# Performance work log

Hardware: AMD Instinct MI355X
Metric: run time of the kernel (lower is better)

The kernel has to match this reference:

```python
import jax, jax.numpy as jnp
import numpy as np

B, S, D, E, K = 2, 2048, 512, 8, 2
H = 4 * D  # 2048


def setup_inputs() -> dict:
    key = jax.random.key(0)
    ks = jax.random.split(key, 6)
    x = jax.random.normal(ks[0], (B, S, D), dtype=jnp.float32)
    # parameters, matching torch init (randn weights, zero biases)
    w1 = jax.random.normal(ks[1], (E, D, H), dtype=jnp.float32)
    w2 = jax.random.normal(ks[2], (E, H, D), dtype=jnp.float32)
    b1 = jnp.zeros((E, H), dtype=jnp.float32)
    b2 = jnp.zeros((E, D), dtype=jnp.float32)
    # nn.Linear(D, E): kaiming-uniform-ish; plain uniform is fine for a baseline
    lim = 1.0 / np.sqrt(D)
    router_w = jax.random.uniform(ks[3], (D, E), dtype=jnp.float32, minval=-lim, maxval=lim)
    router_b = jax.random.uniform(ks[4], (E,), dtype=jnp.float32, minval=-lim, maxval=lim)
    return {"x": x, "w1": w1, "w2": w2, "b1": b1, "b2": b2,
            "router_w": router_w, "router_b": router_b}


def reference(x, w1, w2, b1, b2, router_w, router_b):
    # router: [b,s,e]
    router_logits = jnp.einsum('bsd,de->bse', x, router_w) + router_b
    top_k_logits, top_k_indices = jax.lax.top_k(router_logits, K)   # [b,s,k]
    top_k_probs = jax.nn.softmax(top_k_logits, axis=-1)             # [b,s,k]
    masks = jax.nn.one_hot(top_k_indices, E, dtype=x.dtype)          # [b,s,k,e]
    # dense all-expert MLP (faithful to source: every expert on every token)
    h = jnp.einsum('bsd,edh->bseh', x, w1) + b1                      # [b,s,e,4d]
    h = jax.nn.gelu(h, approximate=False)                            # exact gelu
    y = jnp.einsum('bseh,ehd->bsed', h, w2) + b2                     # [b,s,e,d]
    # combine: mask each expert output by routed prob and sum over top-k
    out = jnp.einsum('bsed,bske,bsk->bsd', y, masks, top_k_probs)    # [b,s,d]
    return out
```

## Files before the change

### kernel.cpp

```cpp
#include <hip/hip_runtime.h>
#include <math.h>

typedef unsigned short u16;
typedef __bf16 bf16x8 __attribute__((ext_vector_type(8)));
typedef float f32x4 __attribute__((ext_vector_type(4)));

#define T_TOKENS 4096
#define D_DIM    512
#define H_DIM    2048
#define E_NUM    8
#define CAP      4096
#define NSLOT    (T_TOKENS * 2)

__device__ __forceinline__ u16 f2bf(float f) {
  unsigned int u = __builtin_bit_cast(unsigned int, f);
  u = (u + 0x7fffu + ((u >> 16) & 1u)) >> 16;
  return (u16)u;
}

__device__ __forceinline__ void gload16(const void* g, void* l) {
  __builtin_amdgcn_global_load_lds(
      (__attribute__((address_space(1))) void*)(g),
      (__attribute__((address_space(3))) void*)(l), 16, 0, 0);
}

__device__ __forceinline__ float gelu_fast(float v) {
  float u = v * __fmaf_rn(0.071354817f, v * v, 1.59576912f);
  float e = __expf(-u);
  return v * __builtin_amdgcn_rcpf(1.0f + e);
}

__global__ __launch_bounds__(256) void transpose_both_kernel(const float* __restrict__ w1,
                                                             const float* __restrict__ w2,
                                                             u16* __restrict__ w1t,
                                                             u16* __restrict__ w2t) {
  __shared__ float tile[64][67];
  int bid = blockIdx.x;
  const float* in; u16* out; int R, C;
  if (bid < 2048) { in = w1; out = w1t; R = D_DIM; C = H_DIM; }
  else            { bid -= 2048; in = w2; out = w2t; R = H_DIM; C = D_DIM; }
  const int e = bid >> 8;
  const int t = bid & 255;
  const int nCx = C >> 6;
  const int c0 = (t % nCx) * 64, r0 = (t / nCx) * 64;
  const float* src = in + (size_t)e * D_DIM * H_DIM;
  u16* dst = out + (size_t)e * D_DIM * H_DIM;
  const int tid = threadIdx.x;
  {
    const int row = tid >> 2, cc = (tid & 3) * 16;
    const float* s = src + (size_t)(r0 + row) * C + c0 + cc;
#pragma unroll
    for (int j = 0; j < 4; j++)
      *(float4*)(&tile[row][cc + 4 * j]) = *(const float4*)(s + 4 * j);
  }
  __syncthreads();
  {
    const int c = tid >> 2, rc = (tid & 3) * 16;
    u16 buf[16];
#pragma unroll
    for (int j = 0; j < 16; j++) buf[j] = f2bf(tile[rc + j][c]);
    u16* d = dst + (size_t)(c0 + c) * R + r0 + rc;
    *(uint4*)(d)     = *(uint4*)(&buf[0]);
    *(uint4*)(d + 8) = *(uint4*)(&buf[8]);
  }
}

__global__ __launch_bounds__(256) void router_kernel(const float* __restrict__ x,
                                                     const float* __restrict__ rw,
                                                     const float* __restrict__ rb,
                                                     int* __restrict__ topk_idx,
                                                     float* __restrict__ topk_p,
                                                     u16* __restrict__ xb,
                                                     float* __restrict__ outz) {
  {
    float4 z = {0.f, 0.f, 0.f, 0.f};
    float4* o = (float4*)(outz + (size_t)blockIdx.x * 2048);
    o[threadIdx.x] = z;
    o[threadIdx.x + 256] = z;
  }
  const int lane = threadIdx.x & 63;
  const int t = blockIdx.x * 4 + (threadIdx.x >> 6);
  const float* xr = x + (size_t)t * D_DIM + lane * 8;
  float xv[8];
  *(float4*)(&xv[0]) = *(const float4*)(xr);
  *(float4*)(&xv[4]) = *(const float4*)(xr + 4);
  ushort4 o0, o1;
  o0.x = f2bf(xv[0]); o0.y = f2bf(xv[1]); o0.z = f2bf(xv[2]); o0.w = f2bf(xv[3]);
  o1.x = f2bf(xv[4]); o1.y = f2bf(xv[5]); o1.z = f2bf(xv[6]); o1.w = f2bf(xv[7]);
  ushort4* xo = (ushort4*)(xb + (size_t)t * D_DIM + lane * 8);
  xo[0] = o0; xo[1] = o1;

  float acc[8] = {0.f,0.f,0.f,0.f,0.f,0.f,0.f,0.f};
#pragma unroll
  for (int j = 0; j < 8; j++) {
    const float4* w = (const float4*)(rw + (size_t)(lane * 8 + j) * E_NUM);
    float4 w0 = w[0], w1 = w[1];
    acc[0] += xv[j] * w0.x; acc[1] += xv[j] * w0.y;
    acc[2] += xv[j] * w0.z; acc[3] += xv[j] * w0.w;
    acc[4] += xv[j] * w1.x; acc[5] += xv[j] * w1.y;
    acc[6] += xv[j] * w1.z; acc[7] += xv[j] * w1.w;
  }
#pragma unroll
  for (int off = 32; off > 0; off >>= 1) {
#pragma unroll
    for (int e = 0; e < 8; e++) acc[e] += __shfl_down(acc[e], off);
  }
  if (lane == 0) {
    float l[8];
#pragma unroll
    for (int e = 0; e < 8; e++) l[e] = acc[e] + rb[e];
    int i0 = 0; float v0 = l[0];
#pragma unroll
    for (int e = 1; e < 8; e++) if (l[e] > v0) { v0 = l[e]; i0 = e; }
    int i1 = -1; float v1 = -3.4e38f;
#pragma unroll
    for (int e = 0; e < 8; e++) if (e != i0 && l[e] > v1) { v1 = l[e]; i1 = e; }
    float p1 = expf(v1 - v0);
    float s = 1.0f + p1;
    topk_idx[t * 2] = i0; topk_idx[t * 2 + 1] = i1;
    topk_p[t * 2] = 1.0f / s; topk_p[t * 2 + 1] = p1 / s;
  }
}

__global__ __launch_bounds__(256) void compact_kernel(const int* __restrict__ topk_idx,
                                                      const float* __restrict__ topk_p,
                                                      int* __restrict__ slot_list,
                                                      float* __restrict__ prob_list,
                                                      int* __restrict__ counts) {
  const int e = blockIdx.x;
  const int tid = threadIdx.x, lane = tid & 63, w = tid >> 6;
  __shared__ int wsum[4];
  __shared__ int sbase;
  if (tid == 0) sbase = 0;
  __syncthreads();
  for (int c0 = 0; c0 < T_TOKENS; c0 += 256) {
    const int t = c0 + tid;
    const int i0 = topk_idx[t * 2], i1 = topk_idx[t * 2 + 1];
    int flag = 0, slot = 0; float p = 0.f;
    if (i0 == e)      { flag = 1; slot = t * 2;     p = topk_p[t * 2]; }
    else if (i1 == e) { flag = 1; slot = t * 2 + 1; p = topk_p[t * 2 + 1]; }
    unsigned long long m = __ballot(flag);
    if (lane == 0) wsum[w] = (int)__popcll(m);
    const int wpre = (int)__popcll(m & ((1ull << lane) - 1ull));
    __syncthreads();
    int base = sbase;
#pragma unroll
    for (int j = 0; j < 4; j++) if (j < w) base += wsum[j];
    const int tot = wsum[0] + wsum[1] + wsum[2] + wsum[3];
    if (flag) { slot_list[e * CAP + base + wpre] = slot; prob_list[e * CAP + base + wpre] = p; }
    __syncthreads();
    if (tid == 0) sbase += tot;
  }
  __syncthreads();
  if (tid == 0) counts[e] = sbase;
}

__global__ __launch_bounds__(256, 2) void gemm1_kernel(const u16* __restrict__ xb,
                                                       const u16* __restrict__ w1t,
                                                       const float* __restrict__ b1,
                                                       const int* __restrict__ slot_list,
                                                       const float* __restrict__ prob_list,
                                                       const int* __restrict__ counts,
                                                       u16* __restrict__ hbuf) {
  const int e  = blockIdx.y >> 5;
  const int rt = blockIdx.y & 31;
  const int cnt = counts[e];
  const int rbase = rt * 128;
  if (rbase >= cnt) return;
  const int n0 = blockIdx.x * 128;

  __shared__ __align__(16) u16 At[2][128 * 64];
  __shared__ __align__(16) u16 Bt[2][128 * 64];

  const int tid = threadIdx.x, lane = tid & 63, wid = tid >> 6;
  const int wr = wid >> 1, wc = wid & 1;
  const int lr8 = lane >> 3;
  const int sx = lane & 7;
  const int kperm = (sx ^ lr8) * 8;
  const int lrow = lane & 15, lk = lane >> 4;

  const u16* pa[4]; const u16* pb[4]; int lo[4];
#pragma unroll
  for (int i = 0; i < 4; i++) {
    const int row = (wid * 4 + i) * 8 + lr8;
    const int grow = rbase + row;
    int tok = 0;
    if (grow < cnt) tok = slot_list[e * CAP + grow] >> 1;
    pa[i] = xb + (size_t)tok * D_DIM + kperm;
    pb[i] = w1t + ((size_t)e * H_DIM + n0 + row) * D_DIM + kperm;
    lo[i] = (wid * 4 + i) * 512;
  }

  f32x4 acc[4][4];
#pragma unroll
  for (int i = 0; i < 4; i++)
#pragma unroll
    for (int j = 0; j < 4; j++) acc[i][j] = (f32x4){0.f, 0.f, 0.f, 0.f};

  auto stage = [&](int k0, int b) {
#pragma unroll
    for (int i = 0; i < 4; i++) gload16(pa[i] + k0, &At[b][lo[i]]);
#pragma unroll
    for (int i = 0; i < 4; i++) gload16(pb[i] + k0, &Bt[b][lo[i]]);
  };

  stage(0, 0);
  stage(64, 1);
  const int nt = D_DIM / 64;
#pragma unroll
  for (int t = 0; t < nt; ++t) {
    const int cur = t & 1;
    if (t < nt - 1) { asm volatile("s_waitcnt vmcnt(8)" ::: "memory"); }
    else            { asm volatile("s_waitcnt vmcnt(0)" ::: "memory"); }
    __builtin_amdgcn_sched_barrier(0);
    __builtin_amdgcn_s_barrier();
    bf16x8 afr[4][2], bfr[4][2];
#pragma unroll
    for (int ks = 0; ks < 2; ks++)
#pragma unroll
      for (int f = 0; f < 4; f++) {
        afr[f][ks] = *(const bf16x8*)(&At[cur][(wr * 64 + f * 16 + lrow) * 64 + ((ks * 4 + lk) ^ sx) * 8]);
        bfr[f][ks] = *(const bf16x8*)(&Bt[cur][(wc * 64 + f * 16 + lrow) * 64 + ((ks * 4 + lk) ^ sx) * 8]);
      }
    asm volatile("s_waitcnt lgkmcnt(0)" ::: "memory");
    __builtin_amdgcn_sched_barrier(0);
    __builtin_amdgcn_s_barrier();
    if (t + 2 < nt) stage((t + 2) * 64, cur);
    __builtin_amdgcn_sched_barrier(0);
    __builtin_amdgcn_s_setprio(1);
#pragma unroll
    for (int ks = 0; ks < 2; ks++)
#pragma unroll
      for (int fr = 0; fr < 4; fr++)
#pragma unroll
        for (int fc = 0; fc < 4; fc++)
          acc[fr][fc] = __builtin_amdgcn_mfma_f32_16x16x32_bf16(afr[fr][ks], bfr[fc][ks], acc[fr][fc], 0, 0, 0);
    __builtin_amdgcn_s_setprio(0);
  }

  float bias[4];
#pragma unroll
  for (int fc = 0; fc < 4; fc++) bias[fc] = b1[e * H_DIM + n0 + wc * 64 + fc * 16 + lrow];
#pragma unroll
  for (int fr = 0; fr < 4; fr++) {
#pragma unroll
    for (int reg = 0; reg < 4; reg++) {
      const int rloc = wr * 64 + fr * 16 + lk * 4 + reg;
      const int grow = rbase + rloc;
      if (grow < cnt) {
        const int slot = slot_list[e * CAP + grow];
        const float p  = prob_list[e * CAP + grow];
        u16* dst = hbuf + (size_t)slot * H_DIM + n0 + wc * 64 + lrow;
#pragma unroll
        for (int fc = 0; fc < 4; fc++) {
          float v = acc[fr][fc][reg] + bias[fc];
          dst[fc * 16] = f2bf(gelu_fast(v) * p);
        }
      }
    }
  }
}

__global__ __launch_bounds__(256, 3) void gemm2_kernel(const u16* __restrict__ hbuf,
                                                       const u16* __restrict__ w2t,
                                                       const float* __restrict__ b2,
                                                       const int* __restrict__ slot_list,
                                                       const float* __restrict__ prob_list,
                                                       const int* __restrict__ counts,
                                                       float* __restrict__ out) {
  const int e  = blockIdx.y >> 6;
  const int rt = blockIdx.y & 63;
  const int cnt = counts[e];
  const int rbase = rt * 64;
  if (rbase >= cnt) return;
  const int n0 = blockIdx.x * 128;

  __shared__ __align__(16) u16 At[2][64 * 64];
  __shared__ __align__(16) u16 Bt[2][128 * 64];

  const int tid = threadIdx.x, lane = tid & 63, wid = tid >> 6;
  const int wr = wid >> 1, wc = wid & 1;
  const int lr8 = lane >> 3;
  const int sx = lane & 7;
  const int kperm = (sx ^ lr8) * 8;
  const int lrow = lane & 15, lk = lane >> 4;

  const u16* pa[2]; int loa[2];
#pragma unroll
  for (int i = 0; i < 2; i++) {
    const int row = (wid * 2 + i) * 8 + lr8;
    const int grow = rbase + row;
    int slot = 0;
    if (grow < cnt) slot = slot_list[e * CAP + grow];
    pa[i] = hbuf + (size_t)slot * H_DIM + kperm;
    loa[i] = (wid * 2 + i) * 512;
  }
  const u16* pb[4]; int lob[4];
#pragma unroll
  for (int i = 0; i < 4; i++) {
    const int row = (wid * 4 + i) * 8 + lr8;
    pb[i] = w2t + ((size_t)e * D_DIM + n0 + row) * H_DIM + kperm;
    lob[i] = (wid * 4 + i) * 512;
  }

  f32x4 acc[2][4];
#pragma unroll
  for (int i = 0; i < 2; i++)
#pragma unroll
    for (int j = 0; j < 4; j++) acc[i][j] = (f32x4){0.f, 0.f, 0.f, 0.f};

  auto stage = [&](int k0, int b) {
#pragma unroll
    for (int i = 0; i < 2; i++) gload16(pa[i] + k0, &At[b][loa[i]]);
#pragma unroll
    for (int i = 0; i < 4; i++) gload16(pb[i] + k0, &Bt[b][lob[i]]);
  };

  stage(0, 0);
  stage(64, 1);
  const int nt = H_DIM / 64;
#pragma unroll 2
  for (int t = 0; t < nt; ++t) {
    const int cur = t & 1;
    if (t < nt - 1) { asm volatile("s_waitcnt vmcnt(6)" ::: "memory"); }
    else            { asm volatile("s_waitcnt vmcnt(0)" ::: "memory"); }
    __builtin_amdgcn_sched_barrier(0);
    __builtin_amdgcn_s_barrier();
    bf16x8 afr[2][2], bfr[4][2];
#pragma unroll
    for (int ks = 0; ks < 2; ks++) {
#pragma unroll
      for (int f = 0; f < 2; f++)
        afr[f][ks] = *(const bf16x8*)(&At[cur][(wr * 32 + f * 16 + lrow) * 64 + ((ks * 4 + lk) ^ sx) * 8]);
#pragma unroll
      for (int f = 0; f < 4; f++)
        bfr[f][ks] = *(const bf16x8*)(&Bt[cur][(wc * 64 + f * 16 + lrow) * 64 + ((ks * 4 + lk) ^ sx) * 8]);
    }
    asm volatile("s_waitcnt lgkmcnt(0)" ::: "memory");
    __builtin_amdgcn_sched_barrier(0);
    __builtin_amdgcn_s_barrier();
    if (t + 2 < nt) stage((t + 2) * 64, cur);
    __builtin_amdgcn_sched_barrier(0);
    __builtin_amdgcn_s_setprio(1);
#pragma unroll
    for (int ks = 0; ks < 2; ks++)
#pragma unroll
      for (int fr = 0; fr < 2; fr++)
#pragma unroll
        for (int fc = 0; fc < 4; fc++)
          acc[fr][fc] = __builtin_amdgcn_mfma_f32_16x16x32_bf16(afr[fr][ks], bfr[fc][ks], acc[fr][fc], 0, 0, 0);
    __builtin_amdgcn_s_setprio(0);
  }

#pragma unroll
  for (int fr = 0; fr < 2; fr++) {
#pragma unroll
    for (int reg = 0; reg < 4; reg++) {
      const int rloc = wr * 32 + fr * 16 + lk * 4 + reg;
      const int grow = rbase + rloc;
      if (grow < cnt) {
        const int slot = slot_list[e * CAP + grow];
        const float p  = prob_list[e * CAP + grow];
        float* dst = out + (size_t)(slot >> 1) * D_DIM + n0 + wc * 64 + lrow;
#pragma unroll
        for (int fc = 0; fc < 4; fc++) {
          float v = acc[fr][fc][reg] + p * b2[e * D_DIM + n0 + wc * 64 + fc * 16 + lrow];
          atomicAdd(&dst[fc * 16], v);
        }
      }
    }
  }
}

extern "C" void kernel_launch(void* const* d_in, const int* in_sizes, int n_in,
                              void* d_out, int out_size, void* d_ws, size_t ws_size,
                              hipStream_t stream) {
  const float* x  = (const float*)d_in[0];
  const float* w1 = (const float*)d_in[1];
  const float* w2 = (const float*)d_in[2];
  const float* b1 = (const float*)d_in[3];
  const float* b2 = (const float*)d_in[4];
  const float* rw = (const float*)d_in[5];
  const float* rb = (const float*)d_in[6];
  float* out = (float*)d_out;

  char* ws = (char*)d_ws;
  size_t off = 0;
  auto alloc = [&](size_t bytes) -> void* {
    void* p = ws + off;
    off = (off + bytes + 255) & ~(size_t)255;
    return p;
  };
  int*   counts    = (int*)alloc(E_NUM * 4);
  int*   slot_list = (int*)alloc((size_t)E_NUM * CAP * 4);
  float* prob_list = (float*)alloc((size_t)E_NUM * CAP * 4);
  int*   topk_idx  = (int*)alloc((size_t)T_TOKENS * 2 * 4);
  float* topk_p    = (float*)alloc((size_t)T_TOKENS * 2 * 4);
  u16*   xb        = (u16*)alloc((size_t)T_TOKENS * D_DIM * 2);
  u16*   w1t       = (u16*)alloc((size_t)E_NUM * H_DIM * D_DIM * 2);
  u16*   w2t       = (u16*)alloc((size_t)E_NUM * H_DIM * D_DIM * 2);
  u16*   hbuf      = (u16*)alloc((size_t)NSLOT * H_DIM * 2);

  transpose_both_kernel<<<4096, 256, 0, stream>>>(w1, w2, w1t, w2t);
  router_kernel<<<T_TOKENS / 4, 256, 0, stream>>>(x, rw, rb, topk_idx, topk_p, xb, out);
  compact_kernel<<<E_NUM, 256, 0, stream>>>(topk_idx, topk_p, slot_list, prob_list, counts);
  gemm1_kernel<<<dim3(H_DIM / 128, E_NUM * 32), 256, 0, stream>>>(xb, w1t, b1, slot_list, prob_list, counts, hbuf);
  gemm2_kernel<<<dim3(D_DIM / 128, E_NUM * 64), 256, 0, stream>>>(hbuf, w2t, b2, slot_list, prob_list, counts, out);
}
```

Measured before the change: 129.0 us.

## Parallelize expert compaction and retile expert GEMMs with triple-buffered pipelines

The serial per-expert compaction kernel is replaced by a chunked count pass plus a parallel scatter pass, so 128 blocks share the work instead of 8 blocks each looping over all tokens. gemm1 moves to 64-row tiles. Both GEMMs get a 3-stage LDS pipeline and a flattened 1D grid that interleaves experts across consecutive blocks. The aim is to cut the serial compaction time, improve load balance across experts and hide more memory latency, at the cost of an extra launch, more LDS per block and lower occupancy for gemm2 (launch bounds 3→2).

Measured after the change: 145.2 us. 12.6% more time.

```diff
diff --git a/kernel.cpp b/kernel.cpp
--- a/kernel.cpp
+++ b/kernel.cpp
@@ -11,6 +11,7 @@
 #define E_NUM    8
 #define CAP      4096
 #define NSLOT    (T_TOKENS * 2)
+#define NCHUNK   16
 
 __device__ __forceinline__ u16 f2bf(float f) {
   unsigned int u = __builtin_bit_cast(unsigned int, f);
@@ -122,37 +123,48 @@
   }
 }
 
-__global__ __launch_bounds__(256) void compact_kernel(const int* __restrict__ topk_idx,
+__global__ __launch_bounds__(256) void count_kernel(const int* __restrict__ topk_idx,
+                                                    int* __restrict__ chunkcnt) {
+  const int b = blockIdx.x, tid = threadIdx.x, lane = tid & 63, w = tid >> 6;
+  const int t = b * 256 + tid;
+  const int i0 = topk_idx[t * 2], i1 = topk_idx[t * 2 + 1];
+  __shared__ int ws[4][E_NUM];
+#pragma unroll
+  for (int e = 0; e < E_NUM; e++) {
+    unsigned long long m = __ballot(i0 == e || i1 == e);
+    if (lane == 0) ws[w][e] = (int)__popcll(m);
+  }
+  __syncthreads();
+  if (tid < E_NUM)
+    chunkcnt[b * E_NUM + tid] = ws[0][tid] + ws[1][tid] + ws[2][tid] + ws[3][tid];
+}
+
+__global__ __launch_bounds__(256) void scatter_kernel(const int* __restrict__ topk_idx,
                                                       const float* __restrict__ topk_p,
+                                                      const int* __restrict__ chunkcnt,
                                                       int* __restrict__ slot_list,
                                                       float* __restrict__ prob_list,
                                                       int* __restrict__ counts) {
-  const int e = blockIdx.x;
+  const int e = blockIdx.x & 7, chunk = blockIdx.x >> 3;
   const int tid = threadIdx.x, lane = tid & 63, w = tid >> 6;
+  int base = 0;
+  for (int c = 0; c < chunk; ++c) base += chunkcnt[c * E_NUM + e];
+  const int t = chunk * 256 + tid;
+  const int i0 = topk_idx[t * 2], i1 = topk_idx[t * 2 + 1];
+  int flag = 0, slot = 0; float p = 0.f;
+  if (i0 == e)      { flag = 1; slot = t * 2;     p = topk_p[t * 2]; }
+  else if (i1 == e) { flag = 1; slot = t * 2 + 1; p = topk_p[t * 2 + 1]; }
+  unsigned long long m = __ballot(flag);
   __shared__ int wsum[4];
-  __shared__ int sbase;
-  if (tid == 0) sbase = 0;
+  if (lane == 0) wsum[w] = (int)__popcll(m);
+  const int wpre = (int)__popcll(m & ((1ull << lane) - 1ull));
   __syncthreads();
-  for (int c0 = 0; c0 < T_TOKENS; c0 += 256) {
-    const int t = c0 + tid;
-    const int i0 = topk_idx[t * 2], i1 = topk_idx[t * 2 + 1];
-    int flag = 0, slot = 0; float p = 0.f;
-    if (i0 == e)      { flag = 1; slot = t * 2;     p = topk_p[t * 2]; }
-    else if (i1 == e) { flag = 1; slot = t * 2 + 1; p = topk_p[t * 2 + 1]; }
-    unsigned long long m = __ballot(flag);
-    if (lane == 0) wsum[w] = (int)__popcll(m);
-    const int wpre = (int)__popcll(m & ((1ull << lane) - 1ull));
-    __syncthreads();
-    int base = sbase;
-#pragma unroll
-    for (int j = 0; j < 4; j++) if (j < w) base += wsum[j];
-    const int tot = wsum[0] + wsum[1] + wsum[2] + wsum[3];
-    if (flag) { slot_list[e * CAP + base + wpre] = slot; prob_list[e * CAP + base + wpre] = p; }
-    __syncthreads();
-    if (tid == 0) sbase += tot;
-  }
-  __syncthreads();
-  if (tid == 0) counts[e] = sbase;
+  int wb = base;
+#pragma unroll
+  for (int j = 0; j < 4; j++) if (j < w) wb += wsum[j];
+  if (flag) { slot_list[e * CAP + wb + wpre] = slot; prob_list[e * CAP + wb + wpre] = p; }
+  if (chunk == NCHUNK - 1 && tid == 0)
+    counts[e] = base + wsum[0] + wsum[1] + wsum[2] + wsum[3];
 }
 
 __global__ __launch_bounds__(256, 2) void gemm1_kernel(const u16* __restrict__ xb,
@@ -162,15 +174,18 @@
                                                        const float* __restrict__ prob_list,
                                                        const int* __restrict__ counts,
                                                        u16* __restrict__ hbuf) {
-  const int e  = blockIdx.y >> 5;
-  const int rt = blockIdx.y & 31;
+  const int f = blockIdx.x;
+  const int e  = f & 7;
+  const int g  = f >> 3;
+  const int cx = g & 15;
+  const int rt = g >> 4;
   const int cnt = counts[e];
-  const int rbase = rt * 128;
+  const int rbase = rt * 64;
   if (rbase >= cnt) return;
-  const int n0 = blockIdx.x * 128;
-
-  __shared__ __align__(16) u16 At[2][128 * 64];
-  __shared__ __align__(16) u16 Bt[2][128 * 64];
+  const int n0 = cx * 128;
+
+  __shared__ __align__(16) u16 At[3][64 * 64];
+  __shared__ __align__(16) u16 Bt[3][128 * 64];
 
   const int tid = threadIdx.x, lane = tid & 63, wid = tid >> 6;
   const int wr = wid >> 1, wc = wid & 1;
@@ -179,73 +194,81 @@
   const int kperm = (sx ^ lr8) * 8;
   const int lrow = lane & 15, lk = lane >> 4;
 
-  const u16* pa[4]; const u16* pb[4]; int lo[4];
-#pragma unroll
-  for (int i = 0; i < 4; i++) {
-    const int row = (wid * 4 + i) * 8 + lr8;
+  const u16* pa[2]; int loa[2];
+#pragma unroll
+  for (int i = 0; i < 2; i++) {
+    const int row = (wid * 2 + i) * 8 + lr8;
     const int grow = rbase + row;
     int tok = 0;
     if (grow < cnt) tok = slot_list[e * CAP + grow] >> 1;
     pa[i] = xb + (size_t)tok * D_DIM + kperm;
+    loa[i] = (wid * 2 + i) * 512;
+  }
+  const u16* pb[4]; int lob[4];
+#pragma unroll
+  for (int i = 0; i < 4; i++) {
+    const int row = (wid * 4 + i) * 8 + lr8;
     pb[i] = w1t + ((size_t)e * H_DIM + n0 + row) * D_DIM + kperm;
-    lo[i] = (wid * 4 + i) * 512;
-  }
-
-  f32x4 acc[4][4];
-#pragma unroll
-  for (int i = 0; i < 4; i++)
+    lob[i] = (wid * 4 + i) * 512;
+  }
+
+  f32x4 acc[2][4];
+#pragma unroll
+  for (int i = 0; i < 2; i++)
 #pragma unroll
     for (int j = 0; j < 4; j++) acc[i][j] = (f32x4){0.f, 0.f, 0.f, 0.f};
 
   auto stage = [&](int k0, int b) {
 #pragma unroll
-    for (int i = 0; i < 4; i++) gload16(pa[i] + k0, &At[b][lo[i]]);
-#pragma unroll
-    for (int i = 0; i < 4; i++) gload16(pb[i] + k0, &Bt[b][lo[i]]);
+    for (int i = 0; i < 2; i++) gload16(pa[i] + k0, &At[b][loa[i]]);
+#pragma unroll
+    for (int i = 0; i < 4; i++) gload16(pb[i] + k0, &Bt[b][lob[i]]);
   };
 
-  stage(0, 0);
-  stage(64, 1);
+  stage(0, 0); stage(64, 1); stage(128, 2);
   const int nt = D_DIM / 64;
-#pragma unroll
+  int cur = 0;
   for (int t = 0; t < nt; ++t) {
-    const int cur = t & 1;
-    if (t < nt - 1) { asm volatile("s_waitcnt vmcnt(8)" ::: "memory"); }
-    else            { asm volatile("s_waitcnt vmcnt(0)" ::: "memory"); }
+    if (t < nt - 2)       { asm volatile("s_waitcnt vmcnt(12)" ::: "memory"); }
+    else if (t == nt - 2) { asm volatile("s_waitcnt vmcnt(6)" ::: "memory"); }
+    else                  { asm volatile("s_waitcnt vmcnt(0)" ::: "memory"); }
     __builtin_amdgcn_sched_barrier(0);
     __builtin_amdgcn_s_barrier();
-    bf16x8 afr[4][2], bfr[4][2];
+    bf16x8 afr[2][2], bfr[4][2];
+#pragma unroll
+    for (int ks = 0; ks < 2; ks++) {
+#pragma unroll
+      for (int fq = 0; fq < 2; fq++)
+        afr[fq][ks] = *(const bf16x8*)(&At[cur][(wr * 32 + fq * 16 + lrow) * 64 + ((ks * 4 + lk) ^ sx) * 8]);
+#pragma unroll
+      for (int fq = 0; fq < 4; fq++)
+        bfr[fq][ks] = *(const bf16x8*)(&Bt[cur][(wc * 64 + fq * 16 + lrow) * 64 + ((ks * 4 + lk) ^ sx) * 8]);
+    }
+    asm volatile("s_waitcnt lgkmcnt(0)" ::: "memory");
+    __builtin_amdgcn_sched_barrier(0);
+    __builtin_amdgcn_s_barrier();
+    if (t + 3 < nt) stage((t + 3) * 64, cur);
+    __builtin_amdgcn_sched_barrier(0);
+    __builtin_amdgcn_s_setprio(1);
 #pragma unroll
     for (int ks = 0; ks < 2; ks++)
 #pragma unroll
-      for (int f = 0; f < 4; f++) {
-        afr[f][ks] = *(const bf16x8*)(&At[cur][(wr * 64 + f * 16 + lrow) * 64 + ((ks * 4 + lk) ^ sx) * 8]);
-        bfr[f][ks] = *(const bf16x8*)(&Bt[cur][(wc * 64 + f * 16 + lrow) * 64 + ((ks * 4 + lk) ^ sx) * 8]);
-      }
-    asm volatile("s_waitcnt lgkmcnt(0)" ::: "memory");
-    __builtin_amdgcn_sched_barrier(0);
-    __builtin_amdgcn_s_barrier();
-    if (t + 2 < nt) stage((t + 2) * 64, cur);
-    __builtin_amdgcn_sched_barrier(0);
-    __builtin_amdgcn_s_setprio(1);
-#pragma unroll
-    for (int ks = 0; ks < 2; ks++)
-#pragma unroll
-      for (int fr = 0; fr < 4; fr++)
+      for (int fr = 0; fr < 2; fr++)
 #pragma unroll
         for (int fc = 0; fc < 4; fc++)
           acc[fr][fc] = __builtin_amdgcn_mfma_f32_16x16x32_bf16(afr[fr][ks], bfr[fc][ks], acc[fr][fc], 0, 0, 0);
     __builtin_amdgcn_s_setprio(0);
+    cur = (cur == 2) ? 0 : cur + 1;
   }
 
   float bias[4];
 #pragma unroll
   for (int fc = 0; fc < 4; fc++) bias[fc] = b1[e * H_DIM + n0 + wc * 64 + fc * 16 + lrow];
 #pragma unroll
-  for (int fr = 0; fr < 4; fr++) {
+  for (int fr = 0; fr < 2; fr++) {
 #pragma unroll
     for (int reg = 0; reg < 4; reg++) {
-      const int rloc = wr * 64 + fr * 16 + lk * 4 + reg;
+      const int rloc = wr * 32 + fr * 16 + lk * 4 + reg;
       const int grow = rbase + rloc;
       if (grow < cnt) {
         const int slot = slot_list[e * CAP + grow];
@@ -261,22 +284,25 @@
   }
 }
 
-__global__ __launch_bounds__(256, 3) void gemm2_kernel(const u16* __restrict__ hbuf,
+__global__ __launch_bounds__(256, 2) void gemm2_kernel(const u16* __restrict__ hbuf,
                                                        const u16* __restrict__ w2t,
                                                        const float* __restrict__ b2,
                                                        const int* __restrict__ slot_list,
                                                        const float* __restrict__ prob_list,
                                                        const int* __restrict__ counts,
                                                        float* __restrict__ out) {
-  const int e  = blockIdx.y >> 6;
-  const int rt = blockIdx.y & 63;
+  const int f = blockIdx.x;
+  const int e  = f & 7;
+  const int g  = f >> 3;
+  const int cx = g & 3;
+  const int rt = g >> 2;
   const int cnt = counts[e];
   const int rbase = rt * 64;
   if (rbase >= cnt) return;
-  const int n0 = blockIdx.x * 128;
-
-  __shared__ __align__(16) u16 At[2][64 * 64];
-  __shared__ __align__(16) u16 Bt[2][128 * 64];
+  const int n0 = cx * 128;
+
+  __shared__ __align__(16) u16 At[3][64 * 64];
+  __shared__ __align__(16) u16 Bt[3][128 * 64];
 
   const int tid = threadIdx.x, lane = tid & 63, wid = tid >> 6;
   const int wr = wid >> 1, wc = wid & 1;
@@ -316,30 +342,29 @@
     for (int i = 0; i < 4; i++) gload16(pb[i] + k0, &Bt[b][lob[i]]);
   };
 
-  stage(0, 0);
-  stage(64, 1);
+  stage(0, 0); stage(64, 1); stage(128, 2);
   const int nt = H_DIM / 64;
-#pragma unroll 2
+  int cur = 0;
   for (int t = 0; t < nt; ++t) {
-    const int cur = t & 1;
-    if (t < nt - 1) { asm volatile("s_waitcnt vmcnt(6)" ::: "memory"); }
-    else            { asm volatile("s_waitcnt vmcnt(0)" ::: "memory"); }
+    if (t < nt - 2)       { asm volatile("s_waitcnt vmcnt(12)" ::: "memory"); }
+    else if (t == nt - 2) { asm volatile("s_waitcnt vmcnt(6)" ::: "memory"); }
+    else                  { asm volatile("s_waitcnt vmcnt(0)" ::: "memory"); }
     __builtin_amdgcn_sched_barrier(0);
     __builtin_amdgcn_s_barrier();
     bf16x8 afr[2][2], bfr[4][2];
 #pragma unroll
     for (int ks = 0; ks < 2; ks++) {
 #pragma unroll
-      for (int f = 0; f < 2; f++)
-        afr[f][ks] = *(const bf16x8*)(&At[cur][(wr * 32 + f * 16 + lrow) * 64 + ((ks * 4 + lk) ^ sx) * 8]);
-#pragma unroll
-      for (int f = 0; f < 4; f++)
-        bfr[f][ks] = *(const bf16x8*)(&Bt[cur][(wc * 64 + f * 16 + lrow) * 64 + ((ks * 4 + lk) ^ sx) * 8]);
+      for (int fq = 0; fq < 2; fq++)
+        afr[fq][ks] = *(const bf16x8*)(&At[cur][(wr * 32 + fq * 16 + lrow) * 64 + ((ks * 4 + lk) ^ sx) * 8]);
+#pragma unroll
+      for (int fq = 0; fq < 4; fq++)
+        bfr[fq][ks] = *(const bf16x8*)(&Bt[cur][(wc * 64 + fq * 16 + lrow) * 64 + ((ks * 4 + lk) ^ sx) * 8]);
     }
     asm volatile("s_waitcnt lgkmcnt(0)" ::: "memory");
     __builtin_amdgcn_sched_barrier(0);
     __builtin_amdgcn_s_barrier();
-    if (t + 2 < nt) stage((t + 2) * 64, cur);
+    if (t + 3 < nt) stage((t + 3) * 64, cur);
     __builtin_amdgcn_sched_barrier(0);
     __builtin_amdgcn_s_setprio(1);
 #pragma unroll
@@ -350,6 +375,7 @@
         for (int fc = 0; fc < 4; fc++)
           acc[fr][fc] = __builtin_amdgcn_mfma_f32_16x16x32_bf16(afr[fr][ks], bfr[fc][ks], acc[fr][fc], 0, 0, 0);
     __builtin_amdgcn_s_setprio(0);
+    cur = (cur == 2) ? 0 : cur + 1;
   }
 
 #pragma unroll
@@ -392,6 +418,7 @@
     return p;
   };
   int*   counts    = (int*)alloc(E_NUM * 4);
+  int*   chunkcnt  = (int*)alloc(NCHUNK * E_NUM * 4);
   int*   slot_list = (int*)alloc((size_t)E_NUM * CAP * 4);
   float* prob_list = (float*)alloc((size_t)E_NUM * CAP * 4);
   int*   topk_idx  = (int*)alloc((size_t)T_TOKENS * 2 * 4);
@@ -403,7 +430,8 @@
 
   transpose_both_kernel<<<4096, 256, 0, stream>>>(w1, w2, w1t, w2t);
   router_kernel<<<T_TOKENS / 4, 256, 0, stream>>>(x, rw, rb, topk_idx, topk_p, xb, out);
-  compact_kernel<<<E_NUM, 256, 0, stream>>>(topk_idx, topk_p, slot_list, prob_list, counts);
-  gemm1_kernel<<<dim3(H_DIM / 128, E_NUM * 32), 256, 0, stream>>>(xb, w1t, b1, slot_list, prob_list, counts, hbuf);
-  gemm2_kernel<<<dim3(D_DIM / 128, E_NUM * 64), 256, 0, stream>>>(hbuf, w2t, b2, slot_list, prob_list, counts, out);
-}
+  count_kernel<<<NCHUNK, 256, 0, stream>>>(topk_idx, chunkcnt);
+  scatter_kernel<<<NCHUNK * E_NUM, 256, 0, stream>>>(topk_idx, topk_p, chunkcnt, slot_list, prob_list, counts);
+  gemm1_kernel<<<E_NUM * 64 * 16, 256, 0, stream>>>(xb, w1t, b1, slot_list, prob_list, counts, hbuf);
+  gemm2_kernel<<<E_NUM * 64 * 4, 256, 0, stream>>>(hbuf, w2t, b2, slot_list, prob_list, counts, out);
+}
```
